# Optimization experiments

Measured on AMD Instinct MI355X. Metric: run time of the kernel, lower is better.

Reference implementation:

```python
import jax, jax.numpy as jnp
import numpy as np

N_HEADS = 16
R = 256.0


def setup_inputs() -> dict:
    key = jax.random.key(0)
    ks = jax.random.split(key, 8)
    B, T, D, H = 4, 1024, 1024, N_HEADS
    s = 1.0 / np.sqrt(D)
    return {
        "x": jax.random.normal(ks[0], (B, T, D), jnp.float32),
        "Wq": jax.random.normal(ks[1], (D, D), jnp.float32) * s,
        "Wk": jax.random.normal(ks[2], (D, D), jnp.float32) * s,
        "Wv": jax.random.normal(ks[3], (D, D), jnp.float32) * s,
        "Wo": jax.random.normal(ks[4], (D, D), jnp.float32) * s,
        "bo": jnp.zeros((D,), jnp.float32),
        "Wspan": jax.random.normal(ks[5], (H, D), jnp.float32) * s,
        "bspan": jnp.zeros((H,), jnp.float32),
    }


def reference(x, Wq, Wk, Wv, Wo, bo, Wspan, bspan):
    B, T, D = x.shape
    H = N_HEADS
    dh = D // H
    scale = jnp.sqrt(jnp.float32(dh))

    # projections -> (B, H, T, dh)
    def proj(W):
        return jnp.einsum('btd,ed->bte', x, W).reshape(B, T, H, dh).transpose(0, 2, 1, 3)
    Q, K, V = proj(Wq), proj(Wk), proj(Wv)

    # learned span per head: z = T * sigmoid(span_net(mean_t x))  -> (B, H)
    z = T * jax.nn.sigmoid(jnp.einsum('bd,hd->bh', x.mean(axis=1), Wspan) + bspan)

    idx = jnp.arange(T, dtype=jnp.float32)
    dist = idx[None, :] - idx[:, None]          # dist[i,j] = j - i
    causal = dist >= 0                           # matches torch code's mask
    dist_c = jnp.maximum(dist, 0.0)

    scores = jnp.einsum('bhtd,bhsd->bhts', Q, K) / scale
    scores = jnp.where(causal[None, None], scores, -jnp.inf)
    attn = jax.nn.softmax(scores, axis=-1)

    # soft span mask chi_z(h) = clamp((R + z - dist)/R, 0, 1)  (Eq 7)
    span_mask = jnp.clip((R + z[:, :, None, None] - dist_c[None, None]) / R, 0.0, 1.0)
    attn = attn * span_mask
    attn = attn / (attn.sum(axis=-1, keepdims=True) + 1e-8)
    # dropout p=0.0 (eval) -> identity

    out = jnp.einsum('bhts,bhsd->bhtd', attn, V)
    out = out.transpose(0, 2, 1, 3).reshape(B, T, D)
    return jnp.einsum('btd,ed->bte', out, Wo) + bo
```

## Files before the change

kernel.cpp:

```cpp
#include <hip/hip_runtime.h>

#define T_SEQ 1024
#define D_MODEL 1024
#define NH 16
#define DH 64
#define R_SPAN 256.0f

typedef unsigned short ushort_t;
typedef __attribute__((ext_vector_type(8))) short bf16x8;
typedef __attribute__((ext_vector_type(4))) float f32x4;

__device__ __forceinline__ ushort_t f2bf(float f){
  union { float f; unsigned u; } v; v.f = f;
  unsigned r = v.u + 0x7fffu + ((v.u >> 16) & 1u);
  return (ushort_t)(r >> 16);
}

__device__ __forceinline__ ushort_t f2bf_fast(float f){
  union { float f; unsigned u; } v; v.f = f;
  return (ushort_t)((v.u + 0x8000u) >> 16);
}

__device__ __forceinline__ float fast_exp2(float x){
#if __has_builtin(__builtin_amdgcn_exp2f)
  return __builtin_amdgcn_exp2f(x);
#else
  return __expf(x * 0.69314718056f);
#endif
}

__device__ __forceinline__ void barrier_lds_only(){
  __builtin_amdgcn_s_waitcnt(0xC07F);
  __builtin_amdgcn_s_barrier();
}

typedef __attribute__((address_space(1))) void GV;
typedef __attribute__((address_space(3))) void LV;
__device__ __forceinline__ void gld16(const void* g, void* l){
  __builtin_amdgcn_global_load_lds((GV*)g, (LV*)l, 16, 0, 0);
}

__global__ void prep_kernel(const float* __restrict__ x,
                            const float* s1, const float* s2, const float* s3, const float* s4,
                            ushort_t* __restrict__ x_bf, ushort_t* __restrict__ w_bf,
                            float* __restrict__ pt){
  const int z = blockIdx.z;
  const int tid = threadIdx.x;

  if (z >= 16){
    const int wz = z - 16;
    const int chunk = wz >> 2;
    const int sub = ((wz & 3) << 4) | (blockIdx.y << 2) | blockIdx.x;
    const float* ws_[4] = {s1, s2, s3, s4};
    const float* src = ws_[chunk] + (size_t)sub * 16384;
    ushort_t* dst = w_bf + ((size_t)chunk << 20) + (size_t)sub * 16384;
#pragma unroll
    for (int i = 0; i < 16; ++i){
      const int o = (i * 256 + tid) * 4;
      float4 v = *(const float4*)(src + o);
      ushort4 u; u.x = f2bf(v.x); u.y = f2bf(v.y); u.z = f2bf(v.z); u.w = f2bf(v.w);
      *(ushort4*)(dst + o) = u;
    }
    return;
  }

  const int dc = blockIdx.x;
  const int b  = blockIdx.y;
  const int tc = z;
  const int dl = tid & 63, tg = tid >> 6;
  const int d = dc * 256 + dl * 4;
  const size_t rowbase = ((size_t)b * T_SEQ + tc * 64 + tg * 16) * D_MODEL + d;
  const float* px = x + rowbase;
  ushort_t* pb = x_bf + rowbase;

  float s0 = 0.f, s1v = 0.f, s2v = 0.f, s3v = 0.f;
#pragma unroll
  for (int tt = 0; tt < 16; ++tt){
    float4 v = *(const float4*)(px + (size_t)tt * D_MODEL);
    ushort4 o; o.x = f2bf(v.x); o.y = f2bf(v.y); o.z = f2bf(v.z); o.w = f2bf(v.w);
    *(ushort4*)(pb + (size_t)tt * D_MODEL) = o;
    s0 += v.x; s1v += v.y; s2v += v.z; s3v += v.w;
  }

  __shared__ float red[4][256];
  *(float4*)&red[tg][dl * 4] = make_float4(s0, s1v, s2v, s3v);
  __syncthreads();
  if (tg == 0){
    float4 a = *(float4*)&red[0][dl * 4];
    float4 c = *(float4*)&red[1][dl * 4];
    float4 e = *(float4*)&red[2][dl * 4];
    float4 g = *(float4*)&red[3][dl * 4];
    float4 t;
    t.x = a.x + c.x + e.x + g.x;
    t.y = a.y + c.y + e.y + g.y;
    t.z = a.z + c.z + e.z + g.z;
    t.w = a.w + c.w + e.w + g.w;
    *(float4*)&pt[((size_t)(tc * 4 + b) << 10) + d] = t;
  }
}

__global__ void span_kernel(const float* __restrict__ pt, const float* __restrict__ Wspan,
                            const float* __restrict__ bspan, float* __restrict__ z){
  const int h = blockIdx.x, b = blockIdx.y, tid = threadIdx.x;
  const float* wv = Wspan + h * D_MODEL;
  float s = 0.f;
  for (int i = tid; i < D_MODEL; i += 256){
    float acc = 0.f;
#pragma unroll
    for (int tc = 0; tc < 16; ++tc) acc += pt[((size_t)(tc * 4 + b) << 10) + i];
    s += acc * wv[i];
  }
  for (int off = 32; off; off >>= 1) s += __shfl_down(s, off, 64);
  __shared__ float r4[4];
  if ((tid & 63) == 0) r4[tid >> 6] = s;
  __syncthreads();
  if (tid == 0){
    float tot = r4[0] + r4[1] + r4[2] + r4[3];
    float logit = tot * (1.0f / T_SEQ) + bspan[h];
    z[b * NH + h] = (float)T_SEQ / (1.0f + __expf(-logit));
  }
}

template<int FP32OUT>
__global__ __launch_bounds__(512) void gemm_bt(
    const ushort_t* __restrict__ A,
    const ushort_t* __restrict__ B,
    void* __restrict__ C,
    const float* __restrict__ bias,
    const int M, const int N, const int K)
{
  __shared__ ushort_t At[2][128 * 32];
  __shared__ ushort_t Bt[2][128 * 32];

  const int z = blockIdx.z;
  const ushort_t* Bz = B + (size_t)z * N * K;

  const int tid = threadIdx.x;
  const int w = tid >> 6, lane = tid & 63;
  const int q = lane >> 4, c = lane & 15;
  const int m0 = blockIdx.y * 128, n0 = blockIdx.x * 128;
  const int wm = (w >> 2) * 64, wn = (w & 3) * 32;

  const int lr = lane >> 2;
  const int lc = (lane & 3) * 8;

  f32x4 acc[4][2] = {};

  const ushort_t* ga0 = A  + (size_t)(m0 + w * 16 + lr) * K + lc;
  const ushort_t* gb0 = Bz + (size_t)(n0 + w * 16 + lr) * K + lc;

  const int S = K >> 5;
  gld16(ga0, &At[0][(w * 16) * 32]);
  gld16(gb0, &Bt[0][(w * 16) * 32]);

  for (int s = 0; s < S; ++s){
    __syncthreads();
    if (s + 1 < S){
      const int k0 = (s + 1) << 5;
      const int nb = (s + 1) & 1;
      gld16(ga0 + k0, &At[nb][(w * 16) * 32]);
      gld16(gb0 + k0, &Bt[nb][(w * 16) * 32]);
    }
    const ushort_t* at = At[s & 1];
    const ushort_t* bt = Bt[s & 1];

    bf16x8 af[4], bfv[2];
#pragma unroll
    for (int i = 0; i < 4; ++i) af[i]  = *(const bf16x8*)&at[(wm + i * 16 + c) * 32 + q * 8];
#pragma unroll
    for (int j = 0; j < 2; ++j) bfv[j] = *(const bf16x8*)&bt[(wn + j * 16 + c) * 32 + q * 8];
#pragma unroll
    for (int i = 0; i < 4; ++i)
#pragma unroll
      for (int j = 0; j < 2; ++j)
        acc[i][j] = __builtin_amdgcn_mfma_f32_16x16x32_bf16(af[i], bfv[j], acc[i][j], 0, 0, 0);
  }

  if (FP32OUT){
#pragma unroll
    for (int i = 0; i < 4; ++i){
#pragma unroll
      for (int j = 0; j < 2; ++j){
        const int row = m0 + wm + i * 16 + q * 4;
        const int col = n0 + wn + j * 16 + c;
#pragma unroll
        for (int r = 0; r < 4; ++r)
          ((float*)C)[(size_t)(row + r) * N + col] = acc[i][j][r] + bias[col];
      }
    }
  } else if (z == 2){
    ushort_t* Cv = (ushort_t*)C + (size_t)2 * M * N;
    const int bb = m0 >> 10;
#pragma unroll
    for (int i = 0; i < 4; ++i){
#pragma unroll
      for (int j = 0; j < 2; ++j){
        const int col = n0 + wn + j * 16 + c;
        const int t0 = (m0 & 1023) + wm + i * 16 + q * 4;
        ushort4 pk;
        pk.x = f2bf_fast(acc[i][j][0]); pk.y = f2bf_fast(acc[i][j][1]);
        pk.z = f2bf_fast(acc[i][j][2]); pk.w = f2bf_fast(acc[i][j][3]);
        *(ushort4*)&Cv[((size_t)bb << 20) + (size_t)col * 1024 + t0] = pk;
      }
    }
  } else {
#pragma unroll
    for (int i = 0; i < 4; ++i){
#pragma unroll
      for (int j = 0; j < 2; ++j){
        const int row = m0 + wm + i * 16 + q * 4;
        const int col = n0 + wn + j * 16 + c;
#pragma unroll
        for (int r = 0; r < 4; ++r)
          ((ushort_t*)C + (size_t)z * M * N)[(size_t)(row + r) * N + col] = f2bf_fast(acc[i][j][r]);
      }
    }
  }
}

#define LP 72
__global__ __launch_bounds__(512) void attn_kernel(
    const ushort_t* __restrict__ Qg,
    const ushort_t* __restrict__ Kg,
    const ushort_t* __restrict__ Vtg,
    const float* __restrict__ zspan,
    ushort_t* __restrict__ Og)
{
  __shared__ ushort_t Qs[128 * LP];
  __shared__ ushort_t Ks[2][64 * LP];
  __shared__ ushort_t Vt[2][64 * LP];
  __shared__ ushort_t Ps[8][16 * LP];

  const int id = blockIdx.x;
  int qt = (id >> 3) & 7;
  if (id >= 256) qt = 7 - qt;
  const int g  = ((id >> 6) << 3) | (id & 7);
  const int b = g >> 4, h = g & 15;
  const int q0 = qt * 128;
  const int tid = threadIdx.x, w = tid >> 6, lane = tid & 63;
  const int q = lane >> 4, c = lane & 15;

  const size_t base = ((size_t)b * T_SEQ) * D_MODEL + (size_t)h * DH;
  const ushort_t* vtb = Vtg + ((size_t)b << 20) + ((size_t)h << 16);

  {
    const int row = tid >> 2, seg = tid & 3;
    const uint4* gq = (const uint4*)(Qg + base + (size_t)(q0 + row) * D_MODEL);
    uint4* qs = (uint4*)&Qs[row * LP];
    qs[seg * 2]     = gq[seg * 2];
    qs[seg * 2 + 1] = gq[seg * 2 + 1];
  }

  const float zz = zspan[b * NH + h];
  const int jend = min(T_SEQ, (int)(q0 + 127 + R_SPAN + zz) + 1);

  f32x4 acc_d = {};
  f32x4 o[4] = {};

  bf16x8 ones8;
#pragma unroll
  for (int i = 0; i < 8; ++i) ones8[i] = (short)0x3F80;

  const int wi0 = q0 + w * 16, wi1 = wi0 + 15;
  int i_row[4];
  float ar4[4];
#pragma unroll
  for (int r = 0; r < 4; ++r){
    i_row[r] = wi0 + q * 4 + r;
    ar4[r] = (R_SPAN + zz + (float)i_row[r]) * (1.0f / R_SPAN);
  }
  float cjR[4];
#pragma unroll
  for (int jf = 0; jf < 4; ++jf) cjR[jf] = (float)(jf * 16 + c) * (1.0f / R_SPAN);
  const float kexp = 0.125f * 1.44269504f;

  const int srow = tid >> 3, sseg = tid & 7;
  const ushort_t* kg = Kg + base + sseg * 8;
  const ushort_t* vg = vtb + (size_t)srow * 1024 + sseg * 8;

  uint4 kreg = *(const uint4*)(kg + (size_t)(q0 + srow) * D_MODEL);
  uint4 vreg = *(const uint4*)(vg + q0);

  __syncthreads();
  const bf16x8 aq0 = *(const bf16x8*)&Qs[(w * 16 + c) * LP + q * 8];
  const bf16x8 aq1 = *(const bf16x8*)&Qs[(w * 16 + c) * LP + 32 + q * 8];

  int it = 0;
  for (int j0 = q0; j0 < jend; j0 += 64, ++it){
    const int buf = it & 1;
    *(uint4*)&Ks[buf][srow * LP + sseg * 8] = kreg;
    *(uint4*)&Vt[buf][srow * LP + sseg * 8] = vreg;
    if (j0 + 64 < jend){
      kreg = *(const uint4*)(kg + (size_t)(j0 + 64 + srow) * D_MODEL);
      vreg = *(const uint4*)(vg + j0 + 64);
    }
    barrier_lds_only();

    if (j0 + 63 < wi0) continue;
    if ((float)(j0 - wi1) > R_SPAN + zz) continue;

    f32x4 s[4] = {};
#pragma unroll
    for (int jf = 0; jf < 4; ++jf){
      bf16x8 bk0 = *(const bf16x8*)&Ks[buf][(jf * 16 + c) * LP + q * 8];
      s[jf] = __builtin_amdgcn_mfma_f32_16x16x32_bf16(aq0, bk0, s[jf], 0, 0, 0);
      bf16x8 bk1 = *(const bf16x8*)&Ks[buf][(jf * 16 + c) * LP + 32 + q * 8];
      s[jf] = __builtin_amdgcn_mfma_f32_16x16x32_bf16(aq1, bk1, s[jf], 0, 0, 0);
    }

    const bool need_mask = (j0 <= wi1);
    const bool full = ((float)(j0 + 63 - wi0) <= zz);

    if (full){
      if (need_mask){
#pragma unroll
        for (int jf = 0; jf < 4; ++jf){
          const int j = j0 + jf * 16 + c;
#pragma unroll
          for (int r = 0; r < 4; ++r){
            float p = fast_exp2(s[jf][r] * kexp);
            p = (j >= i_row[r]) ? p : 0.f;
            Ps[w][(q * 4 + r) * LP + jf * 16 + c] = f2bf_fast(p);
          }
        }
      } else {
#pragma unroll
        for (int jf = 0; jf < 4; ++jf){
#pragma unroll
          for (int r = 0; r < 4; ++r){
            float p = fast_exp2(s[jf][r] * kexp);
            Ps[w][(q * 4 + r) * LP + jf * 16 + c] = f2bf_fast(p);
          }
        }
      }
    } else {
      const float arj = (float)j0 * (1.0f / R_SPAN);
      if (need_mask){
#pragma unroll
        for (int jf = 0; jf < 4; ++jf){
          const int j = j0 + jf * 16 + c;
#pragma unroll
          for (int r = 0; r < 4; ++r){
            float p = fast_exp2(s[jf][r] * kexp);
            p = (j >= i_row[r]) ? p : 0.f;
            float chi = fminf(fmaxf((ar4[r] - arj) - cjR[jf], 0.f), 1.f);
            Ps[w][(q * 4 + r) * LP + jf * 16 + c] = f2bf_fast(p * chi);
          }
        }
      } else {
#pragma unroll
        for (int jf = 0; jf < 4; ++jf){
#pragma unroll
          for (int r = 0; r < 4; ++r){
            float p = fast_exp2(s[jf][r] * kexp);
            float chi = fminf(fmaxf((ar4[r] - arj) - cjR[jf], 0.f), 1.f);
            Ps[w][(q * 4 + r) * LP + jf * 16 + c] = f2bf_fast(p * chi);
          }
        }
      }
    }

    {
      bf16x8 pa0 = *(const bf16x8*)&Ps[w][c * LP + q * 8];
      bf16x8 pa1 = *(const bf16x8*)&Ps[w][c * LP + 32 + q * 8];
      acc_d = __builtin_amdgcn_mfma_f32_16x16x32_bf16(pa0, ones8, acc_d, 0, 0, 0);
      acc_d = __builtin_amdgcn_mfma_f32_16x16x32_bf16(pa1, ones8, acc_d, 0, 0, 0);
#pragma unroll
      for (int nf = 0; nf < 4; ++nf){
        bf16x8 bv0 = *(const bf16x8*)&Vt[buf][(nf * 16 + c) * LP + q * 8];
        o[nf] = __builtin_amdgcn_mfma_f32_16x16x32_bf16(pa0, bv0, o[nf], 0, 0, 0);
        bf16x8 bv1 = *(const bf16x8*)&Vt[buf][(nf * 16 + c) * LP + 32 + q * 8];
        o[nf] = __builtin_amdgcn_mfma_f32_16x16x32_bf16(pa1, bv1, o[nf], 0, 0, 0);
      }
    }
  }

#pragma unroll
  for (int r = 0; r < 4; ++r){
    const float inv = 1.0f / (acc_d[r] + 1e-20f);
    const size_t rowbase = base + (size_t)i_row[r] * D_MODEL;
#pragma unroll
    for (int nf = 0; nf < 4; ++nf){
      Og[rowbase + nf * 16 + c] = f2bf_fast(o[nf][r] * inv);
    }
  }
}

extern "C" void kernel_launch(void* const* d_in, const int* in_sizes, int n_in,
                              void* d_out, int out_size, void* d_ws, size_t ws_size,
                              hipStream_t stream)
{
  const float* x     = (const float*)d_in[0];
  const float* Wq    = (const float*)d_in[1];
  const float* Wk    = (const float*)d_in[2];
  const float* Wv    = (const float*)d_in[3];
  const float* Wo    = (const float*)d_in[4];
  const float* bo    = (const float*)d_in[5];
  const float* Wspan = (const float*)d_in[6];
  const float* bspan = (const float*)d_in[7];

  const size_t MT = (size_t)4 * T_SEQ;

  ushort_t* x_bf = (ushort_t*)d_ws;
  ushort_t* w_bf = x_bf + MT * D_MODEL;
  ushort_t* qkv  = w_bf + (size_t)4 * D_MODEL * D_MODEL;
  ushort_t* attn = qkv + (size_t)3 * MT * D_MODEL;
  float* pt      = (float*)(attn + MT * D_MODEL);
  float* zsp     = pt + 16 * 4 * D_MODEL;

  prep_kernel<<<dim3(4, 4, 32), 256, 0, stream>>>(x, Wq, Wk, Wv, Wo, x_bf, w_bf, pt);
  span_kernel<<<dim3(16, 4), 256, 0, stream>>>(pt, Wspan, bspan, zsp);

  gemm_bt<0><<<dim3(8, 32, 3), 512, 0, stream>>>(x_bf, w_bf, qkv, nullptr, 4096, 1024, 1024);

  attn_kernel<<<dim3(512), 512, 0, stream>>>(qkv, qkv + MT * D_MODEL,
                                             qkv + 2 * MT * D_MODEL, zsp, attn);

  gemm_bt<1><<<dim3(8, 32, 1), 512, 0, stream>>>(attn, w_bf + (size_t)3 * D_MODEL * D_MODEL,
                                                 d_out, bo, 4096, 1024, 1024);
}
```

Baseline: 171.1 us.

## Add dedicated smaller-tile output projection GEMM and MFMA priority hints in attention

```diff
diff --git a/kernel.cpp b/kernel.cpp
--- a/kernel.cpp
+++ b/kernel.cpp
@@ -218,6 +218,72 @@
   }
 }
 
+__global__ __launch_bounds__(256) void gemm_out(
+    const ushort_t* __restrict__ A,
+    const ushort_t* __restrict__ B,
+    float* __restrict__ C,
+    const float* __restrict__ bias,
+    const int M, const int N, const int K)
+{
+  __shared__ ushort_t At[2][64 * 32];
+  __shared__ ushort_t Bt[2][128 * 32];
+
+  const int tid = threadIdx.x;
+  const int w = tid >> 6, lane = tid & 63;
+  const int q = lane >> 4, c = lane & 15;
+  const int m0 = blockIdx.y * 64, n0 = blockIdx.x * 128;
+  const int wn = w * 32;
+
+  const int lr = lane >> 2;
+  const int lc = (lane & 3) * 8;
+
+  f32x4 acc[4][2] = {};
+
+  const ushort_t* ga0 = A + (size_t)(m0 + w * 16 + lr) * K + lc;
+  const ushort_t* gb0 = B + (size_t)(n0 + w * 32 + lr) * K + lc;
+
+  const int S = K >> 5;
+  gld16(ga0,          &At[0][(w * 16) * 32]);
+  gld16(gb0,          &Bt[0][(w * 32) * 32]);
+  gld16(gb0 + 16 * K, &Bt[0][(w * 32 + 16) * 32]);
+
+  for (int s = 0; s < S; ++s){
+    __syncthreads();
+    if (s + 1 < S){
+      const int k0 = (s + 1) << 5;
+      const int nb = (s + 1) & 1;
+      gld16(ga0 + k0,          &At[nb][(w * 16) * 32]);
+      gld16(gb0 + k0,          &Bt[nb][(w * 32) * 32]);
+      gld16(gb0 + 16 * K + k0, &Bt[nb][(w * 32 + 16) * 32]);
+    }
+    const ushort_t* at = At[s & 1];
+    const ushort_t* bt = Bt[s & 1];
+
+    bf16x8 af[4], bfv[2];
+#pragma unroll
+    for (int i = 0; i < 4; ++i) af[i]  = *(const bf16x8*)&at[(i * 16 + c) * 32 + q * 8];
+#pragma unroll
+    for (int j = 0; j < 2; ++j) bfv[j] = *(const bf16x8*)&bt[(wn + j * 16 + c) * 32 + q * 8];
+#pragma unroll
+    for (int i = 0; i < 4; ++i)
+#pragma unroll
+      for (int j = 0; j < 2; ++j)
+        acc[i][j] = __builtin_amdgcn_mfma_f32_16x16x32_bf16(af[i], bfv[j], acc[i][j], 0, 0, 0);
+  }
+
+#pragma unroll
+  for (int i = 0; i < 4; ++i){
+#pragma unroll
+    for (int j = 0; j < 2; ++j){
+      const int row = m0 + i * 16 + q * 4;
+      const int col = n0 + wn + j * 16 + c;
+#pragma unroll
+      for (int r = 0; r < 4; ++r)
+        C[(size_t)(row + r) * N + col] = acc[i][j][r] + bias[col];
+    }
+  }
+}
+
 #define LP 72
 __global__ __launch_bounds__(512) void attn_kernel(
     const ushort_t* __restrict__ Qg,
@@ -300,6 +366,7 @@
     if ((float)(j0 - wi1) > R_SPAN + zz) continue;
 
     f32x4 s[4] = {};
+    __builtin_amdgcn_s_setprio(1);
 #pragma unroll
     for (int jf = 0; jf < 4; ++jf){
       bf16x8 bk0 = *(const bf16x8*)&Ks[buf][(jf * 16 + c) * LP + q * 8];
@@ -307,6 +374,7 @@
       bf16x8 bk1 = *(const bf16x8*)&Ks[buf][(jf * 16 + c) * LP + 32 + q * 8];
       s[jf] = __builtin_amdgcn_mfma_f32_16x16x32_bf16(aq1, bk1, s[jf], 0, 0, 0);
     }
+    __builtin_amdgcn_s_setprio(0);
 
     const bool need_mask = (j0 <= wi1);
     const bool full = ((float)(j0 + 63 - wi0) <= zz);
@@ -363,6 +431,7 @@
     {
       bf16x8 pa0 = *(const bf16x8*)&Ps[w][c * LP + q * 8];
       bf16x8 pa1 = *(const bf16x8*)&Ps[w][c * LP + 32 + q * 8];
+      __builtin_amdgcn_s_setprio(1);
       acc_d = __builtin_amdgcn_mfma_f32_16x16x32_bf16(pa0, ones8, acc_d, 0, 0, 0);
       acc_d = __builtin_amdgcn_mfma_f32_16x16x32_bf16(pa1, ones8, acc_d, 0, 0, 0);
 #pragma unroll
@@ -372,6 +441,7 @@
         bf16x8 bv1 = *(const bf16x8*)&Vt[buf][(nf * 16 + c) * LP + 32 + q * 8];
         o[nf] = __builtin_amdgcn_mfma_f32_16x16x32_bf16(pa1, bv1, o[nf], 0, 0, 0);
       }
+      __builtin_amdgcn_s_setprio(0);
     }
   }
 
@@ -416,6 +486,6 @@
   attn_kernel<<<dim3(512), 512, 0, stream>>>(qkv, qkv + MT * D_MODEL,
                                              qkv + 2 * MT * D_MODEL, zsp, attn);
 
-  gemm_bt<1><<<dim3(8, 32, 1), 512, 0, stream>>>(attn, w_bf + (size_t)3 * D_MODEL * D_MODEL,
-                                                 d_out, bo, 4096, 1024, 1024);
-}
+  gemm_out<<<dim3(8, 64), 256, 0, stream>>>(attn, w_bf + (size_t)3 * D_MODEL * D_MODEL,
+                                            (float*)d_out, bo, 4096, 1024, 1024);
+}
```

Result: no change. 168.1 us (-1.8%).
